# Performance work log

Measured on AMD Instinct MI355X. Metric: run time of the kernel, lower is better.

The kernel has to match this reference:

```python
import jax, jax.numpy as jnp
import numpy as np

N_NODES = 50000
N_EDGES = 640000
F_IN = 64
EDGE_DIM = 16
HID = 128
N_LAYERS = 3
N_CLASSES = 2
NUM_GRAPHS = 64
BN_EPS = 1e-5


def setup_inputs() -> dict:
    key = jax.random.key(0)
    ks = jax.random.split(key, 20)
    s = 0.05
    inp = {
        "x": jax.random.normal(ks[0], (N_NODES, F_IN), dtype=jnp.float32),
        "edge_index": jax.random.randint(ks[1], (2, N_EDGES), 0, N_NODES, dtype=jnp.int32),
        "edge_attr": jax.random.normal(ks[2], (N_EDGES, EDGE_DIM), dtype=jnp.float32),
        "batch": jnp.sort(jax.random.randint(ks[3], (N_NODES,), 0, NUM_GRAPHS, dtype=jnp.int32)),
        # node encoder
        "enc_W": jax.random.normal(ks[4], (F_IN, HID), dtype=jnp.float32) * s,
        "enc_b": jnp.zeros((HID,), dtype=jnp.float32),
        # per-layer GINEConv params (stacked over layers)
        "edge_W": jax.random.normal(ks[5], (N_LAYERS, EDGE_DIM, HID), dtype=jnp.float32) * s,
        "edge_b": jnp.zeros((N_LAYERS, HID), dtype=jnp.float32),
        "mlp_W1": jax.random.normal(ks[6], (N_LAYERS, HID, HID), dtype=jnp.float32) * s,
        "mlp_b1": jnp.zeros((N_LAYERS, HID), dtype=jnp.float32),
        "mlp_W2": jax.random.normal(ks[7], (N_LAYERS, HID, HID), dtype=jnp.float32) * s,
        "mlp_b2": jnp.zeros((N_LAYERS, HID), dtype=jnp.float32),
        "bn_gamma": jnp.ones((N_LAYERS, HID), dtype=jnp.float32),
        "bn_beta": jnp.zeros((N_LAYERS, HID), dtype=jnp.float32),
        # classification head
        "head_W1": jax.random.normal(ks[8], (HID, HID), dtype=jnp.float32) * s,
        "head_b1": jnp.zeros((HID,), dtype=jnp.float32),
        "head_W2": jax.random.normal(ks[9], (HID, N_CLASSES), dtype=jnp.float32) * s,
        "head_b2": jnp.zeros((N_CLASSES,), dtype=jnp.float32),
    }
    return inp


def reference(x, edge_index, edge_attr, batch, enc_W, enc_b, edge_W, edge_b,
              mlp_W1, mlp_b1, mlp_W2, mlp_b2, bn_gamma, bn_beta,
              head_W1, head_b1, head_W2, head_b2):
    src, dst = edge_index[0], edge_index[1]  # message flows src -> dst
    h = x @ enc_W + enc_b  # [N, HID]
    for l in range(N_LAYERS):
        # GINEConv: msg = ReLU(x_src + Lin(edge_attr)); aggr = scatter_add at dst
        e = edge_attr @ edge_W[l] + edge_b[l]          # [E, HID]
        msg = jax.nn.relu(h[src] + e)                  # [E, HID]
        agg = jax.ops.segment_sum(msg, dst, num_segments=N_NODES)
        z = h + agg  # (1 + eps) * x + aggr, eps = 0
        # node MLP: Linear-ReLU-Linear
        z = jax.nn.relu(z @ mlp_W1[l] + mlp_b1[l]) @ mlp_W2[l] + mlp_b2[l]
        # BatchNorm1d (training-mode batch stats) + ReLU (dropout = identity)
        mean = jnp.mean(z, axis=0)
        var = jnp.var(z, axis=0)
        z = bn_gamma[l] * (z - mean) * jax.lax.rsqrt(var + BN_EPS) + bn_beta[l]
        h = jax.nn.relu(z)
    # global_add_pool over graphs
    g = jax.ops.segment_sum(h, batch, num_segments=NUM_GRAPHS)  # [G, HID]
    out = jax.nn.relu(g @ head_W1 + head_b1) @ head_W2 + head_b2
    return out  # [G, N_CLASSES]
```

## Files before the change

kernel.cpp:

```cpp
#include <hip/hip_runtime.h>
#include <hip/hip_bf16.h>

#define N_NODES 50000
#define N_EDGES 640000
#define F_IN 64
#define EDGE_DIM 16
#define HID 128
#define N_LAYERS 3
#define NUM_GRAPHS 64
#define BN_EPS 1e-5f

typedef __attribute__((ext_vector_type(8))) short short8;
typedef __attribute__((ext_vector_type(4))) float f32x4;
typedef __attribute__((ext_vector_type(2))) __fp16 half2v;

__device__ __forceinline__ float bfl(unsigned int u) {
    unsigned int v = u << 16; float f; __builtin_memcpy(&f, &v, 4); return f;
}
__device__ __forceinline__ float bfh(unsigned int u) {
    unsigned int v = u & 0xffff0000u; float f; __builtin_memcpy(&f, &v, 4); return f;
}
__device__ __forceinline__ unsigned int f2bf(float f) {
    unsigned int v; __builtin_memcpy(&v, &f, 4);
    v += 0x7fffu + ((v >> 16) & 1u);
    return v >> 16;
}
__device__ __forceinline__ unsigned int pack2(float lo, float hi) {
    return f2bf(lo) | (f2bf(hi) << 16);
}
__device__ __forceinline__ half2v u2h(unsigned int u) {
    half2v h; __builtin_memcpy(&h, &u, 4); return h;
}
__device__ __forceinline__ unsigned int pkh(float a, float b) {
    half2v h = __builtin_amdgcn_cvt_pkrtz(a, b);
    unsigned int u; __builtin_memcpy(&u, &h, 4); return u;
}

__global__ void k_hist(const int* __restrict__ dst, int* __restrict__ deg) {
    int e = blockIdx.x * 256 + threadIdx.x;
    atomicAdd(&deg[dst[e]], 1);
}

__global__ void k_blockred(const int* __restrict__ deg, int* __restrict__ bsums) {
    __shared__ int s[256];
    int i = blockIdx.x * 256 + threadIdx.x;
    int v = (i < N_NODES) ? deg[i] : 0;
    s[threadIdx.x] = v;
    __syncthreads();
    for (int off = 128; off > 0; off >>= 1) {
        if (threadIdx.x < off) s[threadIdx.x] += s[threadIdx.x + off];
        __syncthreads();
    }
    if (threadIdx.x == 0) bsums[blockIdx.x] = s[0];
}

__global__ void k_scan_bsums(int* __restrict__ bsums, int nb) {
    __shared__ int s[256];
    const int tid = threadIdx.x;
    const int v = (tid < nb) ? bsums[tid] : 0;
    s[tid] = v;
    __syncthreads();
    for (int off = 1; off < 256; off <<= 1) {
        int t = 0;
        if (tid >= off) t = s[tid - off];
        __syncthreads();
        s[tid] += t;
        __syncthreads();
    }
    if (tid < nb) bsums[tid] = s[tid] - v;
}

__global__ void k_scan_blocks(int* __restrict__ deg_rowptr, const int* __restrict__ bsums,
                              int* __restrict__ cursor) {
    __shared__ int s[256];
    int tid = threadIdx.x;
    int i = blockIdx.x * 256 + tid;
    int v = (i < N_NODES) ? deg_rowptr[i] : 0;
    s[tid] = v;
    __syncthreads();
    for (int off = 1; off < 256; off <<= 1) {
        int t = 0;
        if (tid >= off) t = s[tid - off];
        __syncthreads();
        s[tid] += t;
        __syncthreads();
    }
    int excl = s[tid] - v + bsums[blockIdx.x];
    if (i < N_NODES) {
        deg_rowptr[i] = excl;
        cursor[i] = excl;
    }
    if (i == N_NODES - 1) deg_rowptr[N_NODES] = N_EDGES;
}

__global__ void k_fill(const int* __restrict__ dst, int* __restrict__ cursor,
                       int* __restrict__ elist) {
    int e = blockIdx.x * 256 + threadIdx.x;
    int p = atomicAdd(&cursor[dst[e]], 1);
    elist[p] = e;
}

__global__ __launch_bounds__(256) void k_gather(const int* __restrict__ elist,
                                                const int* __restrict__ esrc,
                                                const float* __restrict__ eattr,
                                                int* __restrict__ src_s,
                                                uint4* __restrict__ eattr_h) {
    const int base = blockIdx.x * 1024;
    const int tid = threadIdx.x;
    int p[4], eid[4];
#pragma unroll
    for (int j = 0; j < 4; ++j) p[j] = base + tid + j * 256;
#pragma unroll
    for (int j = 0; j < 4; ++j) eid[j] = elist[p[j]];
    int sv[4];
#pragma unroll
    for (int j = 0; j < 4; ++j) sv[j] = esrc[eid[j]];
    float4 a[4][4];
#pragma unroll
    for (int j = 0; j < 4; ++j) {
        const float* ep = eattr + (size_t)eid[j] * EDGE_DIM;
        a[j][0] = *(const float4*)ep;
        a[j][1] = *(const float4*)(ep + 4);
        a[j][2] = *(const float4*)(ep + 8);
        a[j][3] = *(const float4*)(ep + 12);
    }
#pragma unroll
    for (int j = 0; j < 4; ++j) {
        src_s[p[j]] = sv[j];
        eattr_h[p[j] * 2] = make_uint4(pkh(a[j][0].x, a[j][0].y), pkh(a[j][0].z, a[j][0].w),
                                       pkh(a[j][1].x, a[j][1].y), pkh(a[j][1].z, a[j][1].w));
        eattr_h[p[j] * 2 + 1] = make_uint4(pkh(a[j][2].x, a[j][2].y), pkh(a[j][2].z, a[j][2].w),
                                           pkh(a[j][3].x, a[j][3].y), pkh(a[j][3].z, a[j][3].w));
    }
}

__global__ void k_pack(const float* __restrict__ W1, const float* __restrict__ W2,
                       const float* __restrict__ encW, const float* __restrict__ eW,
                       unsigned short* __restrict__ wp, unsigned short* __restrict__ wpe,
                       unsigned int* __restrict__ wek, float* __restrict__ g,
                       int* __restrict__ row_ptr) {
    const int t = blockIdx.x * 256 + threadIdx.x;
    if (t < 12288) {
        const int mat = t >> 11;
        const int r = t & 2047;
        const int kstep = r >> 9;
        const int ntile = (r >> 6) & 7;
        const int lane = r & 63;
        const float* W = (mat < 3) ? (W1 + mat * 16384) : (W2 + (mat - 3) * 16384);
        const int kbase = kstep * 32 + ((lane >> 4) << 3);
        const int n = ntile * 16 + (lane & 15);
        unsigned int o[4];
#pragma unroll
        for (int jj = 0; jj < 4; ++jj)
            o[jj] = pack2(W[(kbase + 2 * jj) * HID + n], W[(kbase + 2 * jj + 1) * HID + n]);
        *(uint4*)(wp + (size_t)mat * 16384 + (((kstep << 3) + ntile) * 64 + lane) * 8) =
            make_uint4(o[0], o[1], o[2], o[3]);
    } else if (t < 13312) {
        const int r = t - 12288;
        const int kstep = r >> 9;
        const int ntile = (r >> 6) & 7;
        const int lane = r & 63;
        const int kbase = kstep * 32 + ((lane >> 4) << 3);
        const int n = ntile * 16 + (lane & 15);
        unsigned int o[4];
#pragma unroll
        for (int jj = 0; jj < 4; ++jj)
            o[jj] = pack2(encW[(kbase + 2 * jj) * HID + n], encW[(kbase + 2 * jj + 1) * HID + n]);
        *(uint4*)(wpe + (((kstep << 3) + ntile) * 64 + lane) * 8) =
            make_uint4(o[0], o[1], o[2], o[3]);
    } else if (t < 16384) {
        const int r = t - 13312;
        const int l = r >> 10;
        const int rr = r & 1023;
        const int kp = rr >> 7, f = rr & 127;
        const float a = eW[(l * EDGE_DIM + 2 * kp) * HID + f];
        const float b = eW[(l * EDGE_DIM + 2 * kp + 1) * HID + f];
        wek[r] = pkh(a, b);
    } else if (t < 24576) {
        g[t - 16384] = 0.f;
    } else if (t < 24576 + N_NODES + 1) {
        row_ptr[t - 24576] = 0;
    }
}

__global__ __launch_bounds__(256, 3) void k_encm(const float* __restrict__ x,
                                                 const unsigned short* __restrict__ wpe,
                                                 const float* __restrict__ b,
                                                 unsigned short* __restrict__ hb) {
    const int tid = threadIdx.x;
    const int w = tid >> 6, lane = tid & 63;
    const int q = lane >> 4, l15 = lane & 15;
    const int row0 = blockIdx.x * 64 + w * 16;
    const int ar = min(row0 + l15, N_NODES - 1);
    const float* xp = x + (size_t)ar * F_IN + q * 8;
    f32x4 acc[8];
#pragma unroll
    for (int nt = 0; nt < 8; ++nt) acc[nt] = (f32x4){0.f, 0.f, 0.f, 0.f};
#pragma unroll
    for (int ks = 0; ks < 2; ++ks) {
        const float4 v0 = *(const float4*)(xp + ks * 32);
        const float4 v1 = *(const float4*)(xp + ks * 32 + 4);
        unsigned int u[4] = {pack2(v0.x, v0.y), pack2(v0.z, v0.w),
                             pack2(v1.x, v1.y), pack2(v1.z, v1.w)};
        short8 a; __builtin_memcpy(&a, u, 16);
#pragma unroll
        for (int nt = 0; nt < 8; ++nt) {
            const short8 bf = *(const short8*)(wpe + (((ks << 3) + nt) * 64 + lane) * 8);
            acc[nt] = __builtin_amdgcn_mfma_f32_16x16x32_bf16(a, bf, acc[nt], 0, 0, 0);
        }
    }
    const int rowb = row0 + q * 4;
#pragma unroll
    for (int nt = 0; nt < 8; ++nt) {
        const float bias = b[nt * 16 + l15];
        const int cc = nt * 16 + l15;
#pragma unroll
        for (int reg = 0; reg < 4; ++reg) {
            const int r = rowb + reg;
            if (r < N_NODES)
                hb[(size_t)r * HID + cc] = (unsigned short)f2bf(acc[nt][reg] + bias);
        }
    }
}

__global__ __launch_bounds__(256, 2) void k_agg(const unsigned int* __restrict__ in32,
                                                const int* __restrict__ src_s,
                                                const uint4* __restrict__ eattr_h,
                                                const unsigned int* __restrict__ wek,
                                                const float* __restrict__ be,
                                                const int* __restrict__ row_ptr,
                                                const float* __restrict__ bnst,
                                                const float* __restrict__ gamma,
                                                const float* __restrict__ beta,
                                                const int bnmode,
                                                float* __restrict__ bnz,
                                                unsigned int* __restrict__ zb32) {
    if (blockIdx.x == 0) bnz[threadIdx.x] = 0.f;

    const int lane = threadIdx.x & 63;
    const int wv = threadIdx.x >> 6;
    const int f2 = lane * 2;
    half2v wx[8], wy[8];
#pragma unroll
    for (int j = 0; j < 8; ++j) {
        wx[j] = u2h(wek[j * 128 + f2]);
        wy[j] = u2h(wek[j * 128 + f2 + 1]);
    }
    const float2 eb = *(const float2*)&be[f2];

    float2 sc = make_float2(1.f, 1.f), sh = make_float2(0.f, 0.f);
    float rlo = -3.4e38f;
    if (bnmode) {
        const float invN = 1.0f / (float)N_NODES;
        const float m0 = bnst[f2] * invN, m1 = bnst[f2 + 1] * invN;
        const float v0 = fmaxf(bnst[128 + f2] * invN - m0 * m0, 0.f);
        const float v1 = fmaxf(bnst[128 + f2 + 1] * invN - m1 * m1, 0.f);
        const float r0 = rsqrtf(v0 + BN_EPS), r1 = rsqrtf(v1 + BN_EPS);
        sc = make_float2(gamma[f2] * r0, gamma[f2 + 1] * r1);
        sh = make_float2(fmaf(-m0, sc.x, beta[f2]), fmaf(-m1, sc.y, beta[f2 + 1]));
        rlo = 0.f;
    }

    const int n = blockIdx.x * 4 + wv;
    const int base = __builtin_amdgcn_readfirstlane(row_ptr[n]);
    const int deg = __builtin_amdgcn_readfirstlane(row_ptr[n + 1]) - base;

    const unsigned int uself = in32[n * 64 + lane];
    float2 acc = make_float2(fmaxf(fmaf(bfl(uself), sc.x, sh.x), rlo),
                             fmaxf(fmaf(bfh(uself), sc.y, sh.y), rlo));

    if (deg > 0) {
        const int* sp = src_s + base;
        const uint4* ep = eattr_h + (size_t)base * 2;
        const int last = deg - 1;
        const int nch = (deg + 3) >> 2;

        unsigned int huC[4], huN[4];
        uint4 eaC[4][2], eaN[4][2];
        int s2[4];
        {
            int s0[4], s1[4];
#pragma unroll
            for (int j = 0; j < 4; ++j) s0[j] = sp[min(j, last)];
#pragma unroll
            for (int j = 0; j < 4; ++j) huC[j] = in32[s0[j] * 64 + lane];
#pragma unroll
            for (int j = 0; j < 4; ++j) s1[j] = sp[min(4 + j, last)];
            if (nch > 1) {
#pragma unroll
                for (int j = 0; j < 4; ++j) huN[j] = in32[s1[j] * 64 + lane];
            } else {
#pragma unroll
                for (int j = 0; j < 4; ++j) huN[j] = 0u;
            }
#pragma unroll
            for (int j = 0; j < 4; ++j) {
                const int e = min(j, last);
                eaC[j][0] = ep[e * 2]; eaC[j][1] = ep[e * 2 + 1];
            }
#pragma unroll
            for (int j = 0; j < 4; ++j) s2[j] = sp[min(8 + j, last)];
        }
        for (int c = 0; c < nch; ++c) {
            unsigned int huNN[4] = {0u, 0u, 0u, 0u};
            if (c + 2 < nch) {
#pragma unroll
                for (int j = 0; j < 4; ++j) huNN[j] = in32[s2[j] * 64 + lane];
            }
            int s3[4];
#pragma unroll
            for (int j = 0; j < 4; ++j) s3[j] = sp[min((c + 3) * 4 + j, last)];
            if (c + 1 < nch) {
#pragma unroll
                for (int j = 0; j < 4; ++j) {
                    const int e = min((c + 1) * 4 + j, last);
                    eaN[j][0] = ep[e * 2]; eaN[j][1] = ep[e * 2 + 1];
                }
            }
            __builtin_amdgcn_sched_barrier(0);
            const int rem = deg - c * 4;
#pragma unroll
            for (int j = 0; j < 4; ++j) {
                if (j < rem) {
                    const unsigned int* au = (const unsigned int*)&eaC[j][0];
                    float ex = eb.x, ey = eb.y;
#pragma unroll
                    for (int k = 0; k < 8; ++k) {
                        const half2v a = u2h(au[k]);
                        ex = __builtin_amdgcn_fdot2(a, wx[k], ex, false);
                        ey = __builtin_amdgcn_fdot2(a, wy[k], ey, false);
                    }
                    const float hx = fmaxf(fmaf(bfl(huC[j]), sc.x, sh.x), rlo);
                    const float hy = fmaxf(fmaf(bfh(huC[j]), sc.y, sh.y), rlo);
                    acc.x += fmaxf(hx + ex, 0.f);
                    acc.y += fmaxf(hy + ey, 0.f);
                }
            }
            if (c + 1 < nch) {
#pragma unroll
                for (int j = 0; j < 4; ++j) {
                    huC[j] = huN[j]; huN[j] = huNN[j];
                    eaC[j][0] = eaN[j][0]; eaC[j][1] = eaN[j][1];
                    s2[j] = s3[j];
                }
            }
        }
    }
    zb32[n * 64 + lane] = pack2(acc.x, acc.y);
}

#define Z1LD 136

__global__ __launch_bounds__(256, 3) void k_mlp(const unsigned short* __restrict__ zb,
                                                const unsigned short* __restrict__ w1p,
                                                const float* __restrict__ b1,
                                                const unsigned short* __restrict__ w2p,
                                                const float* __restrict__ b2,
                                                unsigned short* __restrict__ z2b,
                                                float* __restrict__ bn) {
    __shared__ unsigned short z1s[64 * Z1LD];
    __shared__ float redA[512];
    __shared__ float redB[512];
    const int tid = threadIdx.x;
    const int w = tid >> 6, lane = tid & 63;
    const int q = lane >> 4, l15 = lane & 15;
    const int row0 = blockIdx.x * 64 + w * 16;

    const int ar = min(row0 + l15, N_NODES - 1);
    const unsigned short* aptr = zb + (size_t)ar * HID + q * 8;

    f32x4 acc[8];
#pragma unroll
    for (int nt = 0; nt < 8; ++nt) acc[nt] = (f32x4){0.f, 0.f, 0.f, 0.f};

#pragma unroll
    for (int ks = 0; ks < 4; ++ks) {
        const short8 a = *(const short8*)(aptr + ks * 32);
#pragma unroll
        for (int nt = 0; nt < 8; ++nt) {
            const short8 b = *(const short8*)(w1p + (((ks << 3) + nt) * 64 + lane) * 8);
            acc[nt] = __builtin_amdgcn_mfma_f32_16x16x32_bf16(a, b, acc[nt], 0, 0, 0);
        }
    }
    {
        const int lr0 = w * 16 + q * 4;
#pragma unroll
        for (int nt = 0; nt < 8; ++nt) {
            const float bias = b1[nt * 16 + l15];
            const int cc = nt * 16 + l15;
#pragma unroll
            for (int reg = 0; reg < 4; ++reg) {
                const float v = fmaxf(acc[nt][reg] + bias, 0.f);
                z1s[(lr0 + reg) * Z1LD + cc] = (unsigned short)f2bf(v);
            }
        }
    }
#pragma unroll
    for (int nt = 0; nt < 8; ++nt) acc[nt] = (f32x4){0.f, 0.f, 0.f, 0.f};
    const unsigned short* a2p = &z1s[(w * 16 + l15) * Z1LD + q * 8];
#pragma unroll
    for (int ks = 0; ks < 4; ++ks) {
        const short8 a = *(const short8*)(a2p + ks * 32);
#pragma unroll
        for (int nt = 0; nt < 8; ++nt) {
            const short8 b = *(const short8*)(w2p + (((ks << 3) + nt) * 64 + lane) * 8);
            acc[nt] = __builtin_amdgcn_mfma_f32_16x16x32_bf16(a, b, acc[nt], 0, 0, 0);
        }
    }
    float s[8], sq[8];
    const int rowb = row0 + q * 4;
#pragma unroll
    for (int nt = 0; nt < 8; ++nt) {
        const float bias = b2[nt * 16 + l15];
        const int cc = nt * 16 + l15;
        float ls = 0.f, lq = 0.f;
#pragma unroll
        for (int reg = 0; reg < 4; ++reg) {
            const int r = rowb + reg;
            const float v = acc[nt][reg] + bias;
            if (r < N_NODES) {
                z2b[(size_t)r * HID + cc] = (unsigned short)f2bf(v);
                ls += v;
                lq = fmaf(v, v, lq);
            }
        }
        s[nt] = ls; sq[nt] = lq;
    }
#pragma unroll
    for (int nt = 0; nt < 8; ++nt) {
        s[nt] += __shfl_xor(s[nt], 16, 64);
        s[nt] += __shfl_xor(s[nt], 32, 64);
        sq[nt] += __shfl_xor(sq[nt], 16, 64);
        sq[nt] += __shfl_xor(sq[nt], 32, 64);
    }
    if (lane < 16) {
#pragma unroll
        for (int nt = 0; nt < 8; ++nt) {
            redA[w * 128 + nt * 16 + lane] = s[nt];
            redB[w * 128 + nt * 16 + lane] = sq[nt];
        }
    }
    __syncthreads();
    if (tid < 128) {
        float t = redA[tid] + redA[128 + tid] + redA[256 + tid] + redA[384 + tid];
        atomicAdd(&bn[tid], t);
    } else {
        const int c = tid - 128;
        float t = redB[c] + redB[128 + c] + redB[256 + c] + redB[384 + c];
        atomicAdd(&bn[128 + c], t);
    }
}

__global__ void k_pool(const unsigned short* __restrict__ z2b, const int* __restrict__ batch,
                       const float* __restrict__ bnst, const float* __restrict__ gamma,
                       const float* __restrict__ beta, float* __restrict__ g) {
    const int f = threadIdx.x;
    const float invN = 1.0f / (float)N_NODES;
    const float m = bnst[f] * invN;
    const float var = fmaxf(bnst[128 + f] * invN - m * m, 0.f);
    const float r = rsqrtf(var + BN_EPS);
    const float sc = gamma[f] * r;
    const float sh = fmaf(-m, sc, beta[f]);

    const int n0 = blockIdx.x * 128;
    const int nend = min(n0 + 128, N_NODES);
    float acc = 0.f;
    int cur = batch[n0];
    for (int n = n0; n < nend; ++n) {
        const int bb = batch[n];
        if (bb != cur) {
            atomicAdd(&g[cur * HID + f], acc);
            acc = 0.f;
            cur = bb;
        }
        const float raw = bfl((unsigned int)z2b[n * HID + f]);
        acc += fmaxf(fmaf(raw, sc, sh), 0.f);
    }
    atomicAdd(&g[cur * HID + f], acc);
}

__global__ __launch_bounds__(1024) void k_head(const float* __restrict__ g,
                                               const float* __restrict__ W1h,
                                               const float* __restrict__ b1h,
                                               const float* __restrict__ W2h,
                                               const float* __restrict__ b2h,
                                               float* __restrict__ out) {
    __shared__ float g1s[NUM_GRAPHS * HID];
    const int tid = threadIdx.x;
#pragma unroll
    for (int i = 0; i < 8; ++i) {
        const int idx = i * 1024 + tid;
        const int r = idx >> 7, c = idx & 127;
        float acc = b1h[c];
        for (int k = 0; k < 128; ++k) acc = fmaf(g[r * HID + k], W1h[k * HID + c], acc);
        g1s[idx] = fmaxf(acc, 0.f);
    }
    __syncthreads();
    if (tid < NUM_GRAPHS * 2) {
        const int r = tid >> 1, c = tid & 1;
        float acc = b2h[c];
        for (int k = 0; k < 128; ++k) acc = fmaf(g1s[r * HID + k], W2h[k * 2 + c], acc);
        out[tid] = acc;
    }
}

extern "C" void kernel_launch(void* const* d_in, const int* in_sizes, int n_in,
                              void* d_out, int out_size, void* d_ws, size_t ws_size,
                              hipStream_t stream) {
    const float* x     = (const float*)d_in[0];
    const int*   ei    = (const int*)d_in[1];
    const float* eattr = (const float*)d_in[2];
    const int*   batch = (const int*)d_in[3];
    const float* encW  = (const float*)d_in[4];
    const float* encb  = (const float*)d_in[5];
    const float* eW    = (const float*)d_in[6];
    const float* eb    = (const float*)d_in[7];
    const float* W1    = (const float*)d_in[8];
    const float* b1    = (const float*)d_in[9];
    const float* W2    = (const float*)d_in[10];
    const float* b2    = (const float*)d_in[11];
    const float* gam   = (const float*)d_in[12];
    const float* bet   = (const float*)d_in[13];
    const float* hW1   = (const float*)d_in[14];
    const float* hb1   = (const float*)d_in[15];
    const float* hW2   = (const float*)d_in[16];
    const float* hb2   = (const float*)d_in[17];
    float* out = (float*)d_out;

    float* ws = (float*)d_ws;
    unsigned short* z2b = (unsigned short*)ws;
    float* bn0 = ws + 3200000;
    float* bn1 = ws + 3200256;
    float* g   = ws + 3200512;
    unsigned short* hb = (unsigned short*)(ws + 3216640);
    unsigned int* zb32 = (unsigned int*)(ws + 6416640);
    int* row_ptr = (int*)(ws + 11216640);
    int* cursor  = row_ptr + N_NODES + 1;
    int* elist   = cursor + N_NODES;
    int* bsums   = elist + N_EDGES;
    int* src_s   = bsums + 256;
    uint4* eattr_h = (uint4*)(ws + 12596900);
    unsigned short* wp  = (unsigned short*)(ws + 17716900);
    unsigned short* wpe = (unsigned short*)(ws + 17766100);
    unsigned int*   wek = (unsigned int*)(ws + 17770200);

    const int* esrc = ei;
    const int* edst = ei + N_EDGES;

    k_pack<<<292, 256, 0, stream>>>(W1, W2, encW, eW, wp, wpe, wek, g, row_ptr);
    k_hist<<<N_EDGES / 256, 256, 0, stream>>>(edst, row_ptr);
    k_blockred<<<196, 256, 0, stream>>>(row_ptr, bsums);
    k_scan_bsums<<<1, 256, 0, stream>>>(bsums, 196);
    k_scan_blocks<<<196, 256, 0, stream>>>(row_ptr, bsums, cursor);
    k_fill<<<N_EDGES / 256, 256, 0, stream>>>(edst, cursor, elist);
    k_gather<<<N_EDGES / 1024, 256, 0, stream>>>(elist, esrc, eattr, src_s, eattr_h);

    k_encm<<<782, 256, 0, stream>>>(x, wpe, encb, hb);

    float* bnbuf[2] = {bn0, bn1};
    for (int l = 0; l < N_LAYERS; ++l) {
        const unsigned int* in32 = (l == 0) ? (const unsigned int*)hb
                                            : (const unsigned int*)z2b;
        float* bnRead = bnbuf[(l + 1) & 1];
        float* bnZero = bnbuf[l & 1];
        k_agg<<<12500, 256, 0, stream>>>(in32, src_s, eattr_h,
                                         wek + l * 1024, eb + l * HID, row_ptr,
                                         bnRead, gam + (l ? (l - 1) * HID : 0),
                                         bet + (l ? (l - 1) * HID : 0),
                                         (l > 0) ? 1 : 0, bnZero, zb32);
        k_mlp<<<782, 256, 0, stream>>>((const unsigned short*)zb32,
                                       wp + (size_t)l * 16384, b1 + l * HID,
                                       wp + (size_t)(3 + l) * 16384, b2 + l * HID,
                                       z2b, bnZero);
    }

    k_pool<<<391, 128, 0, stream>>>(z2b, batch, bn0, gam + 2 * HID, bet + 2 * HID, g);
    k_head<<<1, 1024, 0, stream>>>(g, hW1, hb1, hW2, hb2, out);
}
```

Before: 614.1 us.

## Fuse CSR fill with edge gather, drop sched barrier, vectorize pooling

Merges the edge-list fill and the gather into one kernel. Each edge now reads its own src and attributes coalesced and scatters them directly to its CSR slot, which removes the elist buffer and one launch. It also removes a scheduling barrier in the aggregation loop and rewrites pooling to use 64-thread blocks that each process two bf16 features per 32-bit load. Scattered writes replace scattered reads, and dropping the sched barrier may change how the aggregation kernel's loads overlap with its math.

```diff
diff --git a/kernel.cpp b/kernel.cpp
--- a/kernel.cpp
+++ b/kernel.cpp
@@ -93,45 +93,26 @@
     if (i == N_NODES - 1) deg_rowptr[N_NODES] = N_EDGES;
 }
 
-__global__ void k_fill(const int* __restrict__ dst, int* __restrict__ cursor,
-                       int* __restrict__ elist) {
-    int e = blockIdx.x * 256 + threadIdx.x;
-    int p = atomicAdd(&cursor[dst[e]], 1);
-    elist[p] = e;
-}
-
-__global__ __launch_bounds__(256) void k_gather(const int* __restrict__ elist,
-                                                const int* __restrict__ esrc,
-                                                const float* __restrict__ eattr,
-                                                int* __restrict__ src_s,
-                                                uint4* __restrict__ eattr_h) {
-    const int base = blockIdx.x * 1024;
-    const int tid = threadIdx.x;
-    int p[4], eid[4];
-#pragma unroll
-    for (int j = 0; j < 4; ++j) p[j] = base + tid + j * 256;
-#pragma unroll
-    for (int j = 0; j < 4; ++j) eid[j] = elist[p[j]];
-    int sv[4];
-#pragma unroll
-    for (int j = 0; j < 4; ++j) sv[j] = esrc[eid[j]];
-    float4 a[4][4];
-#pragma unroll
-    for (int j = 0; j < 4; ++j) {
-        const float* ep = eattr + (size_t)eid[j] * EDGE_DIM;
-        a[j][0] = *(const float4*)ep;
-        a[j][1] = *(const float4*)(ep + 4);
-        a[j][2] = *(const float4*)(ep + 8);
-        a[j][3] = *(const float4*)(ep + 12);
-    }
-#pragma unroll
-    for (int j = 0; j < 4; ++j) {
-        src_s[p[j]] = sv[j];
-        eattr_h[p[j] * 2] = make_uint4(pkh(a[j][0].x, a[j][0].y), pkh(a[j][0].z, a[j][0].w),
-                                       pkh(a[j][1].x, a[j][1].y), pkh(a[j][1].z, a[j][1].w));
-        eattr_h[p[j] * 2 + 1] = make_uint4(pkh(a[j][2].x, a[j][2].y), pkh(a[j][2].z, a[j][2].w),
-                                           pkh(a[j][3].x, a[j][3].y), pkh(a[j][3].z, a[j][3].w));
-    }
+__global__ __launch_bounds__(256) void k_fillg(const int* __restrict__ esrc,
+                                               const int* __restrict__ edst,
+                                               const float* __restrict__ eattr,
+                                               int* __restrict__ cursor,
+                                               int* __restrict__ src_s,
+                                               uint4* __restrict__ eattr_h) {
+    const int e = blockIdx.x * 256 + threadIdx.x;
+    const int d = edst[e];
+    const int sv = esrc[e];
+    const float* ep = eattr + (size_t)e * EDGE_DIM;
+    const float4 a0 = *(const float4*)ep;
+    const float4 a1 = *(const float4*)(ep + 4);
+    const float4 a2 = *(const float4*)(ep + 8);
+    const float4 a3 = *(const float4*)(ep + 12);
+    const int p = atomicAdd(&cursor[d], 1);
+    src_s[p] = sv;
+    eattr_h[p * 2] = make_uint4(pkh(a0.x, a0.y), pkh(a0.z, a0.w),
+                                pkh(a1.x, a1.y), pkh(a1.z, a1.w));
+    eattr_h[p * 2 + 1] = make_uint4(pkh(a2.x, a2.y), pkh(a2.z, a2.w),
+                                    pkh(a3.x, a3.y), pkh(a3.z, a3.w));
 }
 
 __global__ void k_pack(const float* __restrict__ W1, const float* __restrict__ W2,
@@ -317,7 +298,6 @@
                     eaN[j][0] = ep[e * 2]; eaN[j][1] = ep[e * 2 + 1];
                 }
             }
-            __builtin_amdgcn_sched_barrier(0);
             const int rem = deg - c * 4;
 #pragma unroll
             for (int j = 0; j < 4; ++j) {
@@ -451,32 +431,41 @@
     }
 }
 
-__global__ void k_pool(const unsigned short* __restrict__ z2b, const int* __restrict__ batch,
-                       const float* __restrict__ bnst, const float* __restrict__ gamma,
-                       const float* __restrict__ beta, float* __restrict__ g) {
+__global__ __launch_bounds__(64) void k_pool(const unsigned int* __restrict__ z2b32,
+                                             const int* __restrict__ batch,
+                                             const float* __restrict__ bnst,
+                                             const float* __restrict__ gamma,
+                                             const float* __restrict__ beta,
+                                             float* __restrict__ g) {
     const int f = threadIdx.x;
+    const int f2 = f * 2;
     const float invN = 1.0f / (float)N_NODES;
-    const float m = bnst[f] * invN;
-    const float var = fmaxf(bnst[128 + f] * invN - m * m, 0.f);
-    const float r = rsqrtf(var + BN_EPS);
-    const float sc = gamma[f] * r;
-    const float sh = fmaf(-m, sc, beta[f]);
-
-    const int n0 = blockIdx.x * 128;
-    const int nend = min(n0 + 128, N_NODES);
-    float acc = 0.f;
+    const float m0 = bnst[f2] * invN, m1 = bnst[f2 + 1] * invN;
+    const float v0 = fmaxf(bnst[128 + f2] * invN - m0 * m0, 0.f);
+    const float v1 = fmaxf(bnst[128 + f2 + 1] * invN - m1 * m1, 0.f);
+    const float r0 = rsqrtf(v0 + BN_EPS), r1 = rsqrtf(v1 + BN_EPS);
+    const float sc0 = gamma[f2] * r0, sc1 = gamma[f2 + 1] * r1;
+    const float sh0 = fmaf(-m0, sc0, beta[f2]), sh1 = fmaf(-m1, sc1, beta[f2 + 1]);
+
+    const int n0 = blockIdx.x * 64;
+    if (n0 >= N_NODES) return;
+    const int nend = min(n0 + 64, N_NODES);
+    float a0 = 0.f, a1 = 0.f;
     int cur = batch[n0];
     for (int n = n0; n < nend; ++n) {
         const int bb = batch[n];
         if (bb != cur) {
-            atomicAdd(&g[cur * HID + f], acc);
-            acc = 0.f;
+            atomicAdd(&g[cur * HID + f2], a0);
+            atomicAdd(&g[cur * HID + f2 + 1], a1);
+            a0 = 0.f; a1 = 0.f;
             cur = bb;
         }
-        const float raw = bfl((unsigned int)z2b[n * HID + f]);
-        acc += fmaxf(fmaf(raw, sc, sh), 0.f);
-    }
-    atomicAdd(&g[cur * HID + f], acc);
+        const unsigned int u = z2b32[n * 64 + f];
+        a0 += fmaxf(fmaf(bfl(u), sc0, sh0), 0.f);
+        a1 += fmaxf(fmaf(bfh(u), sc1, sh1), 0.f);
+    }
+    atomicAdd(&g[cur * HID + f2], a0);
+    atomicAdd(&g[cur * HID + f2 + 1], a1);
 }
 
 __global__ __launch_bounds__(1024) void k_head(const float* __restrict__ g,
@@ -536,8 +525,7 @@
     unsigned int* zb32 = (unsigned int*)(ws + 6416640);
     int* row_ptr = (int*)(ws + 11216640);
     int* cursor  = row_ptr + N_NODES + 1;
-    int* elist   = cursor + N_NODES;
-    int* bsums   = elist + N_EDGES;
+    int* bsums   = cursor + N_NODES;
     int* src_s   = bsums + 256;
     uint4* eattr_h = (uint4*)(ws + 12596900);
     unsigned short* wp  = (unsigned short*)(ws + 17716900);
@@ -552,8 +540,7 @@
     k_blockred<<<196, 256, 0, stream>>>(row_ptr, bsums);
     k_scan_bsums<<<1, 256, 0, stream>>>(bsums, 196);
     k_scan_blocks<<<196, 256, 0, stream>>>(row_ptr, bsums, cursor);
-    k_fill<<<N_EDGES / 256, 256, 0, stream>>>(edst, cursor, elist);
-    k_gather<<<N_EDGES / 1024, 256, 0, stream>>>(elist, esrc, eattr, src_s, eattr_h);
+    k_fillg<<<N_EDGES / 256, 256, 0, stream>>>(esrc, edst, eattr, cursor, src_s, eattr_h);
 
     k_encm<<<782, 256, 0, stream>>>(x, wpe, encb, hb);
 
@@ -574,6 +561,7 @@
                                        z2b, bnZero);
     }
 
-    k_pool<<<391, 128, 0, stream>>>(z2b, batch, bn0, gam + 2 * HID, bet + 2 * HID, g);
+    k_pool<<<782, 64, 0, stream>>>((const unsigned int*)z2b, batch, bn0,
+                                   gam + 2 * HID, bet + 2 * HID, g);
     k_head<<<1, 1024, 0, stream>>>(g, hW1, hb1, hW2, hb2, out);
 }
```

After: 578.1 us. -5.9%, faster.
